# Kernel tuning notes

Measured on AMD Instinct MI355X. Metric: run time of the kernel, lower is better.

The kernel has to match this reference:

```python
import jax, jax.numpy as jnp
import numpy as np

B = 131072
INPUT_SIZE = 128
HIDDEN_SIZE = 128


def setup_inputs() -> dict:
    key = jax.random.key(0)
    ks = jax.random.split(key, 11)
    stdv = 1.0 / (HIDDEN_SIZE ** 0.5)

    def unif(k, shape):
        return jax.random.uniform(k, shape, dtype=jnp.float32, minval=-stdv, maxval=stdv)

    return {
        "x_t": jax.random.normal(ks[0], (B, INPUT_SIZE), dtype=jnp.float32),
        "h_prev": jax.random.normal(ks[1], (B, HIDDEN_SIZE), dtype=jnp.float32),
        "Wz": unif(ks[2], (INPUT_SIZE, HIDDEN_SIZE)),
        "Uz": unif(ks[3], (HIDDEN_SIZE, HIDDEN_SIZE)),
        "bz": unif(ks[4], (HIDDEN_SIZE,)),
        "Wr": unif(ks[5], (INPUT_SIZE, HIDDEN_SIZE)),
        "Ur": unif(ks[6], (HIDDEN_SIZE, HIDDEN_SIZE)),
        "br": unif(ks[7], (HIDDEN_SIZE,)),
        "Wh": unif(ks[8], (INPUT_SIZE, HIDDEN_SIZE)),
        "Uh": unif(ks[9], (HIDDEN_SIZE, HIDDEN_SIZE)),
        "bh": unif(ks[10], (HIDDEN_SIZE,)),
    }


def reference(x_t, h_prev, Wz, Uz, bz, Wr, Ur, br, Wh, Uh, bh):
    # Fuse the three input-side and two hidden-side GEMMs by concatenating weights.
    W = jnp.concatenate([Wz, Wr, Wh], axis=1)        # [I, 3H]
    U = jnp.concatenate([Uz, Ur], axis=1)            # [H, 2H]
    xw = x_t @ W                                     # [B, 3H]
    hu = h_prev @ U                                  # [B, 2H]
    H = bz.shape[0]
    z_t = jax.nn.sigmoid(xw[:, :H] + hu[:, :H] + bz)
    r_t = jax.nn.sigmoid(xw[:, H:2 * H] + hu[:, H:] + br)
    h_cand = jnp.tanh(xw[:, 2 * H:] + (r_t * h_prev) @ Uh + bh)
    h_t = (1.0 - z_t) * h_prev + z_t * h_cand
    return h_t
```

## Files before the change

kernel.cpp:

```cpp
#include <hip/hip_runtime.h>
#include <hip/hip_bf16.h>

typedef __attribute__((ext_vector_type(8))) short bf16x8;
typedef __attribute__((ext_vector_type(4))) float f32x4;

#define GRU_B 131072
#define BM 32
#define TPB 8
#define NBLK (GRU_B / (BM * TPB))

static __device__ __forceinline__ ushort f2bf(float f) {
  union { float f; unsigned u; } v; v.f = f;
  unsigned r = v.u + 0x7FFFu + ((v.u >> 16) & 1u);
  return (ushort)(r >> 16);
}
static __device__ __forceinline__ float bf2f(ushort u) {
  union { unsigned u; float f; } v; v.u = ((unsigned)u) << 16;
  return v.f;
}
static __device__ __forceinline__ unsigned pk2(float a, float b) {
  float2 t; t.x = a; t.y = b;
  __hip_bfloat162 r = __float22bfloat162_rn(t);
  union { __hip_bfloat162 b; unsigned u; } cv; cv.b = r;
  return cv.u;
}
static __device__ __forceinline__ float fsig(float x) {
  return __builtin_amdgcn_rcpf(1.0f + __expf(-x));
}
static __device__ __forceinline__ float ftanh(float x) {
  return 1.0f - 2.0f * __builtin_amdgcn_rcpf(1.0f + __expf(2.0f * x));
}
static __device__ __forceinline__ f32x4 splat4(float s) {
  f32x4 v = {s, s, s, s}; return v;
}

__global__ void wtrans_kernel(const float* __restrict__ wz, const float* __restrict__ uz,
                              const float* __restrict__ wr, const float* __restrict__ ur,
                              const float* __restrict__ wh, const float* __restrict__ uh,
                              ushort* __restrict__ outw) {
  int f = blockIdx.x * 256 + threadIdx.x;
  int mat = f >> 14;
  int rem = f & 16383;
  int chunk = rem >> 9;
  int lane = (rem >> 3) & 63;
  int e = rem & 7;
  int cb = chunk >> 2, k0b = chunk & 3;
  int n = cb * 16 + (lane & 15);
  int k = k0b * 32 + (lane >> 4) * 8 + e;
  const float* src = (mat == 0) ? wz : (mat == 1) ? uz : (mat == 2) ? wr
                   : (mat == 3) ? ur : (mat == 4) ? wh : uh;
  outw[f] = f2bf(src[k * 128 + n]);
}

#define MFMA __builtin_amdgcn_mfma_f32_16x16x32_bf16

__global__ __launch_bounds__(512, 2) void gru_kernel(
    const float* __restrict__ x, const float* __restrict__ hprev,
    const ushort* __restrict__ wt,
    const float* __restrict__ bz, const float* __restrict__ br,
    const float* __restrict__ bh, float* __restrict__ out) {
  __shared__ __align__(16) char smem[24576];
  ushort* xs  = (ushort*)smem;
  ushort* hs  = (ushort*)(smem + 8192);
  ushort* rhs = (ushort*)(smem + 16384);

  const int tid = threadIdx.x;
  const int lane = tid & 63;
  const int wid = tid >> 6;
  const int l15 = lane & 15;
  const int q = lane >> 4;
  const int n0 = wid * 16;

  const float brv = br[n0 + l15];
  const float bzv = bz[n0 + l15];
  const float bhv = bh[n0 + l15];

  const ushort* wlane = wt + (lane << 3);
  bf16x8 W[6][4];
#pragma unroll
  for (int mat = 0; mat < 6; ++mat)
#pragma unroll
    for (int kb = 0; kb < 4; ++kb)
      W[mat][kb] = *(const bf16x8*)(wlane + ((((mat << 3) + wid) << 2) + kb) * 512);

  auto ldsA = [&](const ushort* base, int mr, int k0) -> bf16x8 {
    int row = mr * 16 + l15;
    int bo = (row * 256 + (k0 + q * 8) * 2) ^ ((row & 7) << 4);
    return *(const bf16x8*)((const char*)base + bo);
  };

  const long tile0 = (long)blockIdx.x * TPB;

  float4 px0, px1, ph0, ph1;
  {
    const float4* xg = (const float4*)(x + tile0 * BM * 128);
    const float4* hg = (const float4*)(hprev + tile0 * BM * 128);
    px0 = xg[tid]; px1 = xg[512 + tid];
    ph0 = hg[tid]; ph1 = hg[512 + tid];
  }

  for (int t = 0; t < TPB; ++t) {
    const long row0 = (tile0 + t) * BM;

    {
      int r0 = tid >> 5, cb0 = (tid & 31) << 3;
      int bo0 = (r0 * 256 + cb0) ^ ((r0 & 7) << 4);
      int idx1 = 512 + tid;
      int r1 = idx1 >> 5, cb1 = (idx1 & 31) << 3;
      int bo1 = (r1 * 256 + cb1) ^ ((r1 & 7) << 4);
      uint2 v;
      v.x = pk2(px0.x, px0.y); v.y = pk2(px0.z, px0.w);
      *(uint2*)(smem + bo0) = v;
      v.x = pk2(px1.x, px1.y); v.y = pk2(px1.z, px1.w);
      *(uint2*)(smem + bo1) = v;
      v.x = pk2(ph0.x, ph0.y); v.y = pk2(ph0.z, ph0.w);
      *(uint2*)(smem + 8192 + bo0) = v;
      v.x = pk2(ph1.x, ph1.y); v.y = pk2(ph1.z, ph1.w);
      *(uint2*)(smem + 8192 + bo1) = v;
    }
    __syncthreads();

    f32x4 accr[2];
    accr[0] = splat4(brv); accr[1] = splat4(brv);
#pragma unroll
    for (int kb = 0; kb < 4; ++kb)
#pragma unroll
      for (int mr = 0; mr < 2; ++mr) {
        bf16x8 ax = ldsA(xs, mr, kb * 32);
        bf16x8 ah = ldsA(hs, mr, kb * 32);
        accr[mr] = MFMA(ax, W[2][kb], accr[mr], 0, 0, 0);
        accr[mr] = MFMA(ah, W[3][kb], accr[mr], 0, 0, 0);
      }

#pragma unroll
    for (int mr = 0; mr < 2; ++mr)
#pragma unroll
      for (int j = 0; j < 4; ++j) {
        int row = mr * 16 + q * 4 + j;
        int col = n0 + l15;
        float rv = fsig(accr[mr][j]);
        int bo = (row * 256 + col * 2) ^ ((row & 7) << 4);
        float hp = bf2f(*(const ushort*)((const char*)hs + bo));
        *(ushort*)((char*)rhs + bo) = f2bf(rv * hp);
      }

    __syncthreads();

    if (t + 1 < TPB) {
      const float4* xg = (const float4*)(x + (row0 + BM) * 128);
      const float4* hg = (const float4*)(hprev + (row0 + BM) * 128);
      px0 = xg[tid]; px1 = xg[512 + tid];
      ph0 = hg[tid]; ph1 = hg[512 + tid];
    }

    f32x4 accz[2], acch[2];
    accz[0] = splat4(bzv); accz[1] = splat4(bzv);
    acch[0] = splat4(bhv); acch[1] = splat4(bhv);
#pragma unroll
    for (int kb = 0; kb < 4; ++kb)
#pragma unroll
      for (int mr = 0; mr < 2; ++mr) {
        bf16x8 ax = ldsA(xs, mr, kb * 32);
        bf16x8 ah = ldsA(hs, mr, kb * 32);
        bf16x8 ar = ldsA(rhs, mr, kb * 32);
        accz[mr] = MFMA(ax, W[0][kb], accz[mr], 0, 0, 0);
        accz[mr] = MFMA(ah, W[1][kb], accz[mr], 0, 0, 0);
        acch[mr] = MFMA(ax, W[4][kb], acch[mr], 0, 0, 0);
        acch[mr] = MFMA(ar, W[5][kb], acch[mr], 0, 0, 0);
      }

#pragma unroll
    for (int mr = 0; mr < 2; ++mr)
#pragma unroll
      for (int j = 0; j < 4; ++j) {
        int row = mr * 16 + q * 4 + j;
        int col = n0 + l15;
        float hc = ftanh(acch[mr][j]);
        float zv = fsig(accz[mr][j]);
        int bo = (row * 256 + col * 2) ^ ((row & 7) << 4);
        float hp = bf2f(*(const ushort*)((const char*)hs + bo));
        out[(row0 + row) * 128 + col] = hp + zv * (hc - hp);
      }

    __syncthreads();
  }
}

extern "C" void kernel_launch(void* const* d_in, const int* in_sizes, int n_in,
                              void* d_out, int out_size, void* d_ws, size_t ws_size,
                              hipStream_t stream) {
  const float* x  = (const float*)d_in[0];
  const float* h  = (const float*)d_in[1];
  const float* Wz = (const float*)d_in[2];
  const float* Uz = (const float*)d_in[3];
  const float* bz = (const float*)d_in[4];
  const float* Wr = (const float*)d_in[5];
  const float* Ur = (const float*)d_in[6];
  const float* br = (const float*)d_in[7];
  const float* Wh = (const float*)d_in[8];
  const float* Uh = (const float*)d_in[9];
  const float* bh = (const float*)d_in[10];
  ushort* wt = (ushort*)d_ws;

  hipLaunchKernelGGL(wtrans_kernel, dim3(384), dim3(256), 0, stream,
                     Wz, Uz, Wr, Ur, Wh, Uh, wt);
  hipLaunchKernelGGL(gru_kernel, dim3(NBLK), dim3(512), 0, stream,
                     x, h, wt, bz, br, bh, (float*)d_out);
}
```

Before: 56.89 us.

## Triple-buffer LDS input tiles to drop one barrier and prefetch two tiles ahead

The staged x/h tiles now rotate through three LDS slots and the r*h buffer through two. Each iteration stages the next tile's bf16 data before its own GEMMs, so one __syncthreads per iteration goes away and global loads are issued two tiles ahead. The swizzle also XORs in row bit 3 to cut LDS bank conflicts, and h_prev values are kept in registers for the final blend. LDS use rises to 64KB per block while launch bounds ask for 4 blocks per CU, which may cut achievable occupancy and raise register pressure.

```diff
diff --git a/kernel.cpp b/kernel.cpp
--- a/kernel.cpp
+++ b/kernel.cpp
@@ -32,6 +32,9 @@
 }
 static __device__ __forceinline__ f32x4 splat4(float s) {
   f32x4 v = {s, s, s, s}; return v;
+}
+static __device__ __forceinline__ int swz(int row, int cbyte) {
+  return (row * 256 + cbyte) ^ ((row & 7) << 4) ^ ((row & 8) << 2);
 }
 
 __global__ void wtrans_kernel(const float* __restrict__ wz, const float* __restrict__ uz,
@@ -54,15 +57,12 @@
 
 #define MFMA __builtin_amdgcn_mfma_f32_16x16x32_bf16
 
-__global__ __launch_bounds__(512, 2) void gru_kernel(
+__global__ __launch_bounds__(512, 4) void gru_kernel(
     const float* __restrict__ x, const float* __restrict__ hprev,
     const ushort* __restrict__ wt,
     const float* __restrict__ bz, const float* __restrict__ br,
     const float* __restrict__ bh, float* __restrict__ out) {
-  __shared__ __align__(16) char smem[24576];
-  ushort* xs  = (ushort*)smem;
-  ushort* hs  = (ushort*)(smem + 8192);
-  ushort* rhs = (ushort*)(smem + 16384);
+  __shared__ __align__(16) char smem[65536];
 
   const int tid = threadIdx.x;
   const int lane = tid & 63;
@@ -83,42 +83,47 @@
     for (int kb = 0; kb < 4; ++kb)
       W[mat][kb] = *(const bf16x8*)(wlane + ((((mat << 3) + wid) << 2) + kb) * 512);
 
-  auto ldsA = [&](const ushort* base, int mr, int k0) -> bf16x8 {
+  auto ldsA = [&](const char* base, int mr, int k0) -> bf16x8 {
     int row = mr * 16 + l15;
-    int bo = (row * 256 + (k0 + q * 8) * 2) ^ ((row & 7) << 4);
-    return *(const bf16x8*)((const char*)base + bo);
+    return *(const bf16x8*)(base + swz(row, (k0 + q * 8) * 2));
   };
 
   const long tile0 = (long)blockIdx.x * TPB;
+  const float4* xg = (const float4*)x;
+  const float4* hg = (const float4*)hprev;
+
+  const int r0 = tid >> 5, cb0 = (tid & 31) << 3;
+  const int bo0 = swz(r0, cb0), bo1 = swz(r0 + 16, cb0);
+
+  auto stage = [&](char* S, const float4& a0, const float4& a1,
+                   const float4& b0, const float4& b1) {
+    uint2 v;
+    v.x = pk2(a0.x, a0.y); v.y = pk2(a0.z, a0.w); *(uint2*)(S + bo0) = v;
+    v.x = pk2(a1.x, a1.y); v.y = pk2(a1.z, a1.w); *(uint2*)(S + bo1) = v;
+    v.x = pk2(b0.x, b0.y); v.y = pk2(b0.z, b0.w); *(uint2*)(S + 8192 + bo0) = v;
+    v.x = pk2(b1.x, b1.y); v.y = pk2(b1.z, b1.w); *(uint2*)(S + 8192 + bo1) = v;
+  };
 
   float4 px0, px1, ph0, ph1;
   {
-    const float4* xg = (const float4*)(x + tile0 * BM * 128);
-    const float4* hg = (const float4*)(hprev + tile0 * BM * 128);
-    px0 = xg[tid]; px1 = xg[512 + tid];
-    ph0 = hg[tid]; ph1 = hg[512 + tid];
+    long toff = tile0 * 1024;
+    px0 = xg[toff + tid]; px1 = xg[toff + 512 + tid];
+    ph0 = hg[toff + tid]; ph1 = hg[toff + 512 + tid];
+    stage(smem, px0, px1, ph0, ph1);
+    if (TPB > 1) {
+      toff += 1024;
+      px0 = xg[toff + tid]; px1 = xg[toff + 512 + tid];
+      ph0 = hg[toff + tid]; ph1 = hg[toff + 512 + tid];
+    }
   }
+  __syncthreads();
 
   for (int t = 0; t < TPB; ++t) {
+    char* Scur = smem + (t % 3) * 16384;
+    char* RHc  = smem + 49152 + (t & 1) * 8192;
     const long row0 = (tile0 + t) * BM;
 
-    {
-      int r0 = tid >> 5, cb0 = (tid & 31) << 3;
-      int bo0 = (r0 * 256 + cb0) ^ ((r0 & 7) << 4);
-      int idx1 = 512 + tid;
-      int r1 = idx1 >> 5, cb1 = (idx1 & 31) << 3;
-      int bo1 = (r1 * 256 + cb1) ^ ((r1 & 7) << 4);
-      uint2 v;
-      v.x = pk2(px0.x, px0.y); v.y = pk2(px0.z, px0.w);
-      *(uint2*)(smem + bo0) = v;
-      v.x = pk2(px1.x, px1.y); v.y = pk2(px1.z, px1.w);
-      *(uint2*)(smem + bo1) = v;
-      v.x = pk2(ph0.x, ph0.y); v.y = pk2(ph0.z, ph0.w);
-      *(uint2*)(smem + 8192 + bo0) = v;
-      v.x = pk2(ph1.x, ph1.y); v.y = pk2(ph1.z, ph1.w);
-      *(uint2*)(smem + 8192 + bo1) = v;
-    }
-    __syncthreads();
+    if (t + 1 < TPB) stage(smem + ((t + 1) % 3) * 16384, px0, px1, ph0, ph1);
 
     f32x4 accr[2];
     accr[0] = splat4(brv); accr[1] = splat4(brv);
@@ -126,32 +131,23 @@
     for (int kb = 0; kb < 4; ++kb)
 #pragma unroll
       for (int mr = 0; mr < 2; ++mr) {
-        bf16x8 ax = ldsA(xs, mr, kb * 32);
-        bf16x8 ah = ldsA(hs, mr, kb * 32);
-        accr[mr] = MFMA(ax, W[2][kb], accr[mr], 0, 0, 0);
-        accr[mr] = MFMA(ah, W[3][kb], accr[mr], 0, 0, 0);
-      }
-
+        accr[mr] = MFMA(ldsA(Scur, mr, kb * 32), W[2][kb], accr[mr], 0, 0, 0);
+        accr[mr] = MFMA(ldsA(Scur + 8192, mr, kb * 32), W[3][kb], accr[mr], 0, 0, 0);
+      }
+
+    float hpv[2][4];
 #pragma unroll
     for (int mr = 0; mr < 2; ++mr)
 #pragma unroll
       for (int j = 0; j < 4; ++j) {
         int row = mr * 16 + q * 4 + j;
-        int col = n0 + l15;
-        float rv = fsig(accr[mr][j]);
-        int bo = (row * 256 + col * 2) ^ ((row & 7) << 4);
-        float hp = bf2f(*(const ushort*)((const char*)hs + bo));
-        *(ushort*)((char*)rhs + bo) = f2bf(rv * hp);
+        int bo = swz(row, (n0 + l15) * 2);
+        float hp = bf2f(*(const ushort*)(Scur + 8192 + bo));
+        hpv[mr][j] = hp;
+        *(ushort*)(RHc + bo) = f2bf(fsig(accr[mr][j]) * hp);
       }
 
     __syncthreads();
-
-    if (t + 1 < TPB) {
-      const float4* xg = (const float4*)(x + (row0 + BM) * 128);
-      const float4* hg = (const float4*)(hprev + (row0 + BM) * 128);
-      px0 = xg[tid]; px1 = xg[512 + tid];
-      ph0 = hg[tid]; ph1 = hg[512 + tid];
-    }
 
     f32x4 accz[2], acch[2];
     accz[0] = splat4(bzv); accz[1] = splat4(bzv);
@@ -160,9 +156,9 @@
     for (int kb = 0; kb < 4; ++kb)
 #pragma unroll
       for (int mr = 0; mr < 2; ++mr) {
-        bf16x8 ax = ldsA(xs, mr, kb * 32);
-        bf16x8 ah = ldsA(hs, mr, kb * 32);
-        bf16x8 ar = ldsA(rhs, mr, kb * 32);
+        bf16x8 ax = ldsA(Scur, mr, kb * 32);
+        bf16x8 ah = ldsA(Scur + 8192, mr, kb * 32);
+        bf16x8 ar = ldsA(RHc, mr, kb * 32);
         accz[mr] = MFMA(ax, W[0][kb], accz[mr], 0, 0, 0);
         accz[mr] = MFMA(ah, W[1][kb], accz[mr], 0, 0, 0);
         acch[mr] = MFMA(ax, W[4][kb], acch[mr], 0, 0, 0);
@@ -174,15 +170,17 @@
 #pragma unroll
       for (int j = 0; j < 4; ++j) {
         int row = mr * 16 + q * 4 + j;
-        int col = n0 + l15;
         float hc = ftanh(acch[mr][j]);
         float zv = fsig(accz[mr][j]);
-        int bo = (row * 256 + col * 2) ^ ((row & 7) << 4);
-        float hp = bf2f(*(const ushort*)((const char*)hs + bo));
-        out[(row0 + row) * 128 + col] = hp + zv * (hc - hp);
-      }
-
-    __syncthreads();
+        float hp = hpv[mr][j];
+        out[(row0 + row) * 128 + n0 + l15] = hp + zv * (hc - hp);
+      }
+
+    if (t + 2 < TPB) {
+      long toff = (tile0 + t + 2) * 1024;
+      px0 = xg[toff + tid]; px1 = xg[toff + 512 + tid];
+      ph0 = hg[toff + tid]; ph1 = hg[toff + 512 + tid];
+    }
   }
 }
 
```

Measured after the change: 136.9 us. 2.41x slower.
